# Kernel optimization log

Measured on AMD Instinct MI355X. Metric: run time of the kernel, lower is better.

Reference implementation:

```python
import jax, jax.numpy as jnp
import numpy as np

TOPK = 13
NUM_CLASSES = 80
ALPHA = 1.0
BETA = 6.0
EPS = 1e-9
IOU_EPS = 1e-6  # mmdet BboxOverlaps2D union clamp


def setup_inputs() -> dict:
    key = jax.random.key(0)
    k0, k1, k2, k3, k4 = jax.random.split(key, 5)
    B, G, C = 32, 64, NUM_CLASSES
    # Prior center points for a 640x640 image, strides 8/16/32 -> 8400 priors.
    pts = []
    for s in (8, 16, 32):
        n = 640 // s
        xs = (jnp.arange(n, dtype=jnp.float32) + 0.5) * s
        gy, gx = jnp.meshgrid(xs, xs, indexing='ij')
        pts.append(jnp.stack([gx.ravel(), gy.ravel()], axis=-1))
    priors_points = jnp.concatenate(pts, axis=0)  # [8400, 2]
    P = priors_points.shape[0]
    pred_scores = jax.random.uniform(k0, (B, P, C), dtype=jnp.float32)
    half = jax.random.uniform(k1, (B, P, 2), minval=8.0, maxval=64.0)
    pred_bboxes = jnp.concatenate([priors_points[None] - half,
                                   priors_points[None] + half], axis=-1)
    xy = jax.random.uniform(k2, (B, G, 2), minval=0.0, maxval=560.0)
    wh = jax.random.uniform(k3, (B, G, 2), minval=16.0, maxval=80.0)
    gt_bboxes = jnp.concatenate([xy, xy + wh], axis=-1)
    gt_labels = jax.random.randint(k4, (B, G, 1), 0, C).astype(jnp.int64)
    pad_bbox_flag = jnp.ones((B, G, 1), jnp.float32)
    return {
        'pred_scores': pred_scores,
        'pred_bboxes': pred_bboxes,
        'priors_points': priors_points,
        'gt_labels': gt_labels,
        'gt_bboxes': gt_bboxes,
        'pad_bbox_flag': pad_bbox_flag,
    }


def _pairwise_iou(gt_bboxes, pred_bboxes):
    # gt [B,G,4], pred [B,P,4] (xyxy) -> IoU [B,G,P]
    lt = jnp.maximum(gt_bboxes[:, :, None, :2], pred_bboxes[:, None, :, :2])
    rb = jnp.minimum(gt_bboxes[:, :, None, 2:], pred_bboxes[:, None, :, 2:])
    wh = jnp.clip(rb - lt, 0.0)
    inter = wh[..., 0] * wh[..., 1]
    area_g = (gt_bboxes[..., 2] - gt_bboxes[..., 0]) * (gt_bboxes[..., 3] - gt_bboxes[..., 1])
    area_p = (pred_bboxes[..., 2] - pred_bboxes[..., 0]) * (pred_bboxes[..., 3] - pred_bboxes[..., 1])
    union = area_g[:, :, None] + area_p[:, None, :] - inter
    return inter / jnp.maximum(union, IOU_EPS)


def _assign(pred_scores, pred_bboxes, priors_points, gt_labels, gt_bboxes, pad_bbox_flag):
    B, P, C = pred_scores.shape
    G = gt_bboxes.shape[1]
    labels = gt_labels[..., 0].astype(jnp.int32)  # [B,G]

    # --- box metrics ---
    ps = jnp.swapaxes(pred_scores, 1, 2)  # [B,C,P]
    bbox_scores = ps[jnp.arange(B)[:, None], labels, :]  # [B,G,P]
    overlaps = _pairwise_iou(gt_bboxes, pred_bboxes)      # [B,G,P]
    align = (bbox_scores ** ALPHA) * (overlaps ** BETA)   # [B,G,P]

    # --- candidates inside gt boxes ---
    deltas = jnp.concatenate([
        priors_points[None, None] - gt_bboxes[:, :, None, :2],
        gt_bboxes[:, :, None, 2:] - priors_points[None, None]], axis=-1)  # [B,G,P,4]
    mask_in_gts = (deltas.min(axis=-1) > EPS).astype(align.dtype)  # [B,G,P]

    # --- topk candidate selection ---
    metrics = align * mask_in_gts
    _, topk_idxs = jax.lax.top_k(metrics, TOPK)  # [B,G,TOPK]
    topk_mask = (pad_bbox_flag > 0)              # [B,G,1], broadcasts over TOPK
    topk_idxs = jnp.where(topk_mask, topk_idxs, 0)
    flat_idx = topk_idxs.reshape(B * G, TOPK)
    counts = jnp.zeros((B * G, P), metrics.dtype)
    counts = counts.at[jnp.arange(B * G)[:, None], flat_idx].add(1.0)
    counts = counts.reshape(B, G, P)
    is_in_topk = jnp.where(counts > 1, 0.0, counts)
    pos_mask = is_in_topk * mask_in_gts * pad_bbox_flag  # [B,G,P]

    # --- resolve priors matched to multiple gts: keep highest-IoU gt ---
    fg_mask = pos_mask.sum(axis=1)  # [B,P]
    multi = fg_mask[:, None, :] > 1  # [B,1,P] -> broadcasts to [B,G,P]
    max_ov_idx = overlaps.argmax(axis=1)  # [B,P]
    is_max = jnp.swapaxes(jax.nn.one_hot(max_ov_idx, G, dtype=pos_mask.dtype), 1, 2)  # [B,G,P]
    pos_mask = jnp.where(multi, is_max, pos_mask)
    fg_mask = pos_mask.sum(axis=1)          # [B,P]
    assigned_gt_inds = pos_mask.argmax(axis=1)  # [B,P]

    # --- gather targets ---
    flat_gt = assigned_gt_inds + jnp.arange(B)[:, None] * G  # [B,P]
    assigned_labels = jnp.maximum(labels.reshape(-1)[flat_gt], 0)  # [B,P]
    assigned_bboxes = gt_bboxes.reshape(-1, 4)[flat_gt]            # [B,P,4]
    assigned_scores = jax.nn.one_hot(assigned_labels, C, dtype=pred_scores.dtype)
    assigned_scores = jnp.where((fg_mask > 0)[..., None], assigned_scores, 0.0)

    # --- normalize scores by alignment metric ---
    am = align * pos_mask
    pos_align = am.max(axis=-1, keepdims=True)                 # [B,G,1]
    pos_over = (overlaps * pos_mask).max(axis=-1, keepdims=True)
    norm = (am * pos_over / (pos_align + EPS)).max(axis=1)[..., None]  # [B,P,1]
    assigned_scores = assigned_scores * norm

    return assigned_labels, assigned_bboxes, assigned_scores, fg_mask > 0


def reference(pred_scores, pred_bboxes, priors_points, gt_labels, gt_bboxes, pad_bbox_flag):
    return _assign(pred_scores, pred_bboxes, priors_points, gt_labels, gt_bboxes, pad_bbox_flag)
```

## Files before the change

### kernel.cpp

```cpp
#include <hip/hip_runtime.h>
#include <cstdint>

#pragma clang fp contract(off)

#define B_ 32
#define G_ 64
#define C_ 80
#define P_ 8400
#define TOPK_ 13
#define EPS_IN 1e-9f
#define IOU_EPS_ 1e-6f

typedef unsigned long long u64;
typedef unsigned int u32;

__device__ __forceinline__ float iou_pair(float g0, float g1, float g2, float g3,
                                          float p0, float p1, float p2, float p3) {
    float ix1 = fmaxf(g0, p0);
    float iy1 = fmaxf(g1, p1);
    float ix2 = fminf(g2, p2);
    float iy2 = fminf(g3, p3);
    float iw = fmaxf(ix2 - ix1, 0.0f);
    float ih = fmaxf(iy2 - iy1, 0.0f);
    float inter = iw * ih;
    float ag = (g2 - g0) * (g3 - g1);
    float ap = (p2 - p0) * (p3 - p1);
    float uni = ag + ap - inter;
    return inter / fmaxf(uni, IOU_EPS_);
}

__device__ __forceinline__ float pow6(float x) {
    float x2 = x * x;
    float x4 = x2 * x2;
    return x4 * x2;
}

__global__ __launch_bounds__(256) void topk_kernel(
    const float* __restrict__ pred_scores,
    const float* __restrict__ pred_bboxes,
    const float* __restrict__ priors,
    const int* __restrict__ gt_labels,
    const float* __restrict__ gt_bboxes,
    const float* __restrict__ pad_flag,
    int* __restrict__ cnt,
    int* __restrict__ gsel0)
{
    const int wave = threadIdx.x >> 6;
    const int lane = threadIdx.x & 63;
    const int g = blockIdx.x * 4 + wave;
    const int b = blockIdx.y;
    if (pad_flag[b * G_ + g] <= 0.0f) return;

    const float g0 = gt_bboxes[(b * G_ + g) * 4 + 0];
    const float g1 = gt_bboxes[(b * G_ + g) * 4 + 1];
    const float g2 = gt_bboxes[(b * G_ + g) * 4 + 2];
    const float g3 = gt_bboxes[(b * G_ + g) * 4 + 3];
    int lab = gt_labels[b * G_ + g];
    lab = lab < 0 ? 0 : (lab > C_ - 1 ? C_ - 1 : lab);

    const float4* pb = (const float4*)(pred_bboxes + (size_t)b * P_ * 4);
    const float2* pp = (const float2*)priors;
    const float* ps = pred_scores + (size_t)b * P_ * C_ + lab;

    int x0_[3], y0_[3], nx_[3], c_[3], n_[3] = {80, 40, 20}, base_[3] = {0, 6400, 8000};
    {
        const float invs[3] = {0.125f, 0.0625f, 0.03125f};
#pragma unroll
        for (int l = 0; l < 3; ++l) {
            int n = n_[l];
            int x0 = (int)floorf(g0 * invs[l] - 0.5f) - 1;
            int x1 = (int)ceilf (g2 * invs[l] - 0.5f) + 1;
            int y0 = (int)floorf(g1 * invs[l] - 0.5f) - 1;
            int y1 = (int)ceilf (g3 * invs[l] - 0.5f) + 1;
            x0 = x0 < 0 ? 0 : x0;  y0 = y0 < 0 ? 0 : y0;
            x1 = x1 > n - 1 ? n - 1 : x1;  y1 = y1 > n - 1 ? n - 1 : y1;
            int nx = x1 - x0 + 1, ny = y1 - y0 + 1;
            x0_[l] = x0; y0_[l] = y0;
            nx_[l] = nx > 0 ? nx : 1;
            c_[l] = (nx > 0 && ny > 0) ? nx * ny : 0;
        }
    }
    const int c0 = c_[0], c01 = c_[0] + c_[1], total = c01 + c_[2];

    u64 k0 = 0, k1 = 0, k2 = 0, k3 = 0, k4 = 0, k5 = 0;

    for (int j = lane; j < total; j += 64) {
        int l = (j >= c0) + (j >= c01);
        int r = j - (l == 0 ? 0 : (l == 1 ? c0 : c01));
        int nx = l == 0 ? nx_[0] : (l == 1 ? nx_[1] : nx_[2]);
        int n  = l == 0 ? 80 : (l == 1 ? 40 : 20);
        int bs = l == 0 ? 0 : (l == 1 ? 6400 : 8000);
        int x0 = l == 0 ? x0_[0] : (l == 1 ? x0_[1] : x0_[2]);
        int y0 = l == 0 ? y0_[0] : (l == 1 ? y0_[1] : y0_[2]);
        int iy = r / nx;
        int ix = r - iy * nx;
        int p = bs + (y0 + iy) * n + (x0 + ix);

        float2 pt = pp[p];
        float d0 = pt.x - g0, d1 = pt.y - g1;
        float d2 = g2 - pt.x, d3 = g3 - pt.y;
        float mn = fminf(fminf(d0, d1), fminf(d2, d3));
        if (mn > EPS_IN) {
            float4 box = pb[p];
            float iou = iou_pair(g0, g1, g2, g3, box.x, box.y, box.z, box.w);
            float m = ps[(size_t)p * C_] * pow6(iou);
            u64 key = ((u64)__float_as_uint(m) << 32) | (u32)(~(u32)p);
            bool b0 = key > k0, b1 = key > k1, b2 = key > k2,
                 b3 = key > k3, b4 = key > k4, b5 = key > k5;
            k5 = b4 ? k4 : (b5 ? key : k5);
            k4 = b3 ? k3 : (b4 ? key : k4);
            k3 = b2 ? k2 : (b3 ? key : k3);
            k2 = b1 ? k1 : (b2 ? key : k2);
            k1 = b0 ? k0 : (b1 ? key : k1);
            k0 = b0 ? key : k0;
        }
    }

    u64 mykey = 0;
#pragma unroll
    for (int r = 0; r < TOPK_; ++r) {
        u64 m = k0;
#pragma unroll
        for (int off = 1; off < 64; off <<= 1) {
            u64 o = __shfl_xor(m, off, 64);
            m = o > m ? o : m;
        }
        if (lane == r) mykey = m;
        if (k0 == m && m != 0) {
            k0 = k1; k1 = k2; k2 = k3; k3 = k4; k4 = k5; k5 = 0;
        }
    }

    if (lane < TOPK_ && mykey != 0) {
        int p = (int)(~(u32)mykey);
        atomicAdd(&cnt[b * P_ + p], 1);
        gsel0[b * P_ + p] = g;
    }
}

__global__ __launch_bounds__(256) void assign_kernel(
    const float* __restrict__ pred_scores,
    const float* __restrict__ pred_bboxes,
    const int* __restrict__ gt_labels,
    const float* __restrict__ gt_bboxes,
    const int* __restrict__ cnt,
    int* __restrict__ gsel,
    int* __restrict__ labout,
    float* __restrict__ alignv,
    int* __restrict__ pos_align,
    int* __restrict__ pos_over,
    float* __restrict__ out)
{
    const int b = blockIdx.y;
    const int p = blockIdx.x * 256 + threadIdx.x;
    __shared__ float sgt[G_ * 4];
    __shared__ int slab[G_];
    if (threadIdx.x < G_ * 4) sgt[threadIdx.x] = gt_bboxes[b * G_ * 4 + threadIdx.x];
    if (threadIdx.x < G_) slab[threadIdx.x] = gt_labels[b * G_ + threadIdx.x];
    __syncthreads();
    if (p >= P_) return;

    const int bp = b * P_ + p;
    float4 box = ((const float4*)pred_bboxes)[(size_t)b * P_ + p];

    int c = cnt[bp];
    int g = -1;
    if (c == 1) {
        g = gsel[bp];
    } else if (c > 1) {
        float best = -1.0f;
        int bi = 0;
        for (int gg = 0; gg < G_; ++gg) {
            float v = iou_pair(sgt[gg * 4], sgt[gg * 4 + 1], sgt[gg * 4 + 2], sgt[gg * 4 + 3],
                               box.x, box.y, box.z, box.w);
            if (v > best) { best = v; bi = gg; }
        }
        g = bi;
    }
    gsel[bp] = g;

    const int gu = g < 0 ? 0 : g;
    int labraw = slab[gu];
    int labc = labraw < 0 ? 0 : labraw;

    float* out_lab = out;
    float4* out_bbox = (float4*)(out + (size_t)B_ * P_);
    float* out_fg = out + (size_t)B_ * P_ * (size_t)(1 + 4 + C_);

    out_lab[bp] = (float)labc;
    out_bbox[bp] = make_float4(sgt[gu * 4], sgt[gu * 4 + 1], sgt[gu * 4 + 2], sgt[gu * 4 + 3]);
    out_fg[bp] = g >= 0 ? 1.0f : 0.0f;

    if (g >= 0) {
        float iou = iou_pair(sgt[g * 4], sgt[g * 4 + 1], sgt[g * 4 + 2], sgt[g * 4 + 3],
                             box.x, box.y, box.z, box.w);
        int lb = labc > C_ - 1 ? C_ - 1 : labc;
        float s = pred_scores[(size_t)bp * C_ + lb];
        float al = s * pow6(iou);
        alignv[bp] = al;
        labout[bp] = lb;
        atomicMax(&pos_align[b * G_ + g], __float_as_int(al));
        atomicMax(&pos_over[b * G_ + g], __float_as_int(iou));
    }
}

__global__ __launch_bounds__(256) void scores_fill_kernel(
    const int* __restrict__ gsel,
    const int* __restrict__ labout,
    const float* __restrict__ alignv,
    const int* __restrict__ pos_align,
    const int* __restrict__ pos_over,
    float* __restrict__ out_scores)
{
    int bp = blockIdx.x * 256 + threadIdx.x;
    if (bp >= B_ * P_) return;
    int g = gsel[bp];
    if (g < 0) return;
    int b = bp / P_;
    int bg = b * G_ + g;
    float pa = __int_as_float(pos_align[bg]);
    float po = __int_as_float(pos_over[bg]);
    float val = alignv[bp] * po / (pa + 1e-9f);
    out_scores[(size_t)bp * C_ + labout[bp]] = val;
}

extern "C" void kernel_launch(void* const* d_in, const int* in_sizes, int n_in,
                              void* d_out, int out_size, void* d_ws, size_t ws_size,
                              hipStream_t stream) {
    (void)in_sizes; (void)n_in; (void)out_size; (void)ws_size;
    const float* pred_scores = (const float*)d_in[0];
    const float* pred_bboxes = (const float*)d_in[1];
    const float* priors      = (const float*)d_in[2];
    const int*   gt_labels   = (const int*)d_in[3];
    const float* gt_bboxes   = (const float*)d_in[4];
    const float* pad_flag    = (const float*)d_in[5];
    float* out = (float*)d_out;

    char* ws = (char*)d_ws;
    const size_t BP = (size_t)B_ * P_;
    const size_t BG = (size_t)B_ * G_;
    int* cnt       = (int*)ws;
    int* pos_align = (int*)(ws + BP * 4);
    int* pos_over  = (int*)(ws + BP * 4 + BG * 4);
    int* gsel      = (int*)(ws + BP * 4 + 2 * BG * 4);
    int* labout    = gsel + BP;
    float* alignv  = (float*)(labout + BP);

    hipMemsetAsync(ws, 0, (BP + 2 * BG) * 4, stream);
    hipMemsetAsync(out + BP * 5, 0, BP * (size_t)C_ * 4, stream);

    topk_kernel<<<dim3(G_ / 4, B_), 256, 0, stream>>>(
        pred_scores, pred_bboxes, priors, gt_labels, gt_bboxes, pad_flag, cnt, gsel);

    assign_kernel<<<dim3((P_ + 255) / 256, B_), 256, 0, stream>>>(
        pred_scores, pred_bboxes, gt_labels, gt_bboxes, cnt, gsel, labout, alignv,
        pos_align, pos_over, out);

    scores_fill_kernel<<<(int)((BP + 255) / 256), 256, 0, stream>>>(
        gsel, labout, alignv, pos_align, pos_over, out + BP * 5);
}
```

Measured before the change: 191.7 us.

## Fuse memsets and three kernels into one cooperative kernel with grid syncs

Replaces the two memsets and the three kernel launches with a single cooperative kernel of 512 blocks that zeroes the workspace and score output, runs the per-GT top-k, assigns priors, and fills normalized scores, with grid-wide syncs between phases. Per-prior assignment results are held in registers across the last grid sync instead of being written to and re-read from workspace arrays. The aim is to remove launch and memset overheads and the intermediate global traffic. In exchange it adds grid.sync costs, reads GT boxes from global memory instead of shared memory, and limits parallelism to a fixed grid in the zeroing and top-k phases.

```diff
diff --git a/kernel.cpp b/kernel.cpp
--- a/kernel.cpp
+++ b/kernel.cpp
@@ -1,7 +1,10 @@
 #include <hip/hip_runtime.h>
+#include <hip/hip_cooperative_groups.h>
 #include <cstdint>
 
 #pragma clang fp contract(off)
+
+namespace cg = cooperative_groups;
 
 #define B_ 32
 #define G_ 64
@@ -10,6 +13,8 @@
 #define TOPK_ 13
 #define EPS_IN 1e-9f
 #define IOU_EPS_ 1e-6f
+#define NBLK_ 512
+#define NTHR_ (NBLK_ * 256)
 
 typedef unsigned long long u64;
 typedef unsigned int u32;
@@ -35,7 +40,7 @@
     return x4 * x2;
 }
 
-__global__ __launch_bounds__(256) void topk_kernel(
+__global__ __launch_bounds__(256, 2) void fused_kernel(
     const float* __restrict__ pred_scores,
     const float* __restrict__ pred_bboxes,
     const float* __restrict__ priors,
@@ -43,185 +48,188 @@
     const float* __restrict__ gt_bboxes,
     const float* __restrict__ pad_flag,
     int* __restrict__ cnt,
-    int* __restrict__ gsel0)
-{
-    const int wave = threadIdx.x >> 6;
-    const int lane = threadIdx.x & 63;
-    const int g = blockIdx.x * 4 + wave;
-    const int b = blockIdx.y;
-    if (pad_flag[b * G_ + g] <= 0.0f) return;
-
-    const float g0 = gt_bboxes[(b * G_ + g) * 4 + 0];
-    const float g1 = gt_bboxes[(b * G_ + g) * 4 + 1];
-    const float g2 = gt_bboxes[(b * G_ + g) * 4 + 2];
-    const float g3 = gt_bboxes[(b * G_ + g) * 4 + 3];
-    int lab = gt_labels[b * G_ + g];
-    lab = lab < 0 ? 0 : (lab > C_ - 1 ? C_ - 1 : lab);
-
-    const float4* pb = (const float4*)(pred_bboxes + (size_t)b * P_ * 4);
-    const float2* pp = (const float2*)priors;
-    const float* ps = pred_scores + (size_t)b * P_ * C_ + lab;
-
-    int x0_[3], y0_[3], nx_[3], c_[3], n_[3] = {80, 40, 20}, base_[3] = {0, 6400, 8000};
-    {
-        const float invs[3] = {0.125f, 0.0625f, 0.03125f};
-#pragma unroll
-        for (int l = 0; l < 3; ++l) {
-            int n = n_[l];
-            int x0 = (int)floorf(g0 * invs[l] - 0.5f) - 1;
-            int x1 = (int)ceilf (g2 * invs[l] - 0.5f) + 1;
-            int y0 = (int)floorf(g1 * invs[l] - 0.5f) - 1;
-            int y1 = (int)ceilf (g3 * invs[l] - 0.5f) + 1;
-            x0 = x0 < 0 ? 0 : x0;  y0 = y0 < 0 ? 0 : y0;
-            x1 = x1 > n - 1 ? n - 1 : x1;  y1 = y1 > n - 1 ? n - 1 : y1;
-            int nx = x1 - x0 + 1, ny = y1 - y0 + 1;
-            x0_[l] = x0; y0_[l] = y0;
-            nx_[l] = nx > 0 ? nx : 1;
-            c_[l] = (nx > 0 && ny > 0) ? nx * ny : 0;
-        }
-    }
-    const int c0 = c_[0], c01 = c_[0] + c_[1], total = c01 + c_[2];
-
-    u64 k0 = 0, k1 = 0, k2 = 0, k3 = 0, k4 = 0, k5 = 0;
-
-    for (int j = lane; j < total; j += 64) {
-        int l = (j >= c0) + (j >= c01);
-        int r = j - (l == 0 ? 0 : (l == 1 ? c0 : c01));
-        int nx = l == 0 ? nx_[0] : (l == 1 ? nx_[1] : nx_[2]);
-        int n  = l == 0 ? 80 : (l == 1 ? 40 : 20);
-        int bs = l == 0 ? 0 : (l == 1 ? 6400 : 8000);
-        int x0 = l == 0 ? x0_[0] : (l == 1 ? x0_[1] : x0_[2]);
-        int y0 = l == 0 ? y0_[0] : (l == 1 ? y0_[1] : y0_[2]);
-        int iy = r / nx;
-        int ix = r - iy * nx;
-        int p = bs + (y0 + iy) * n + (x0 + ix);
-
-        float2 pt = pp[p];
-        float d0 = pt.x - g0, d1 = pt.y - g1;
-        float d2 = g2 - pt.x, d3 = g3 - pt.y;
-        float mn = fminf(fminf(d0, d1), fminf(d2, d3));
-        if (mn > EPS_IN) {
-            float4 box = pb[p];
-            float iou = iou_pair(g0, g1, g2, g3, box.x, box.y, box.z, box.w);
-            float m = ps[(size_t)p * C_] * pow6(iou);
-            u64 key = ((u64)__float_as_uint(m) << 32) | (u32)(~(u32)p);
-            bool b0 = key > k0, b1 = key > k1, b2 = key > k2,
-                 b3 = key > k3, b4 = key > k4, b5 = key > k5;
-            k5 = b4 ? k4 : (b5 ? key : k5);
-            k4 = b3 ? k3 : (b4 ? key : k4);
-            k3 = b2 ? k2 : (b3 ? key : k3);
-            k2 = b1 ? k1 : (b2 ? key : k2);
-            k1 = b0 ? k0 : (b1 ? key : k1);
-            k0 = b0 ? key : k0;
-        }
-    }
-
-    u64 mykey = 0;
-#pragma unroll
-    for (int r = 0; r < TOPK_; ++r) {
-        u64 m = k0;
-#pragma unroll
-        for (int off = 1; off < 64; off <<= 1) {
-            u64 o = __shfl_xor(m, off, 64);
-            m = o > m ? o : m;
-        }
-        if (lane == r) mykey = m;
-        if (k0 == m && m != 0) {
-            k0 = k1; k1 = k2; k2 = k3; k3 = k4; k4 = k5; k5 = 0;
-        }
-    }
-
-    if (lane < TOPK_ && mykey != 0) {
-        int p = (int)(~(u32)mykey);
-        atomicAdd(&cnt[b * P_ + p], 1);
-        gsel0[b * P_ + p] = g;
-    }
-}
-
-__global__ __launch_bounds__(256) void assign_kernel(
-    const float* __restrict__ pred_scores,
-    const float* __restrict__ pred_bboxes,
-    const int* __restrict__ gt_labels,
-    const float* __restrict__ gt_bboxes,
-    const int* __restrict__ cnt,
-    int* __restrict__ gsel,
-    int* __restrict__ labout,
-    float* __restrict__ alignv,
+    int* __restrict__ gsel0,
     int* __restrict__ pos_align,
     int* __restrict__ pos_over,
     float* __restrict__ out)
 {
-    const int b = blockIdx.y;
-    const int p = blockIdx.x * 256 + threadIdx.x;
-    __shared__ float sgt[G_ * 4];
-    __shared__ int slab[G_];
-    if (threadIdx.x < G_ * 4) sgt[threadIdx.x] = gt_bboxes[b * G_ * 4 + threadIdx.x];
-    if (threadIdx.x < G_) slab[threadIdx.x] = gt_labels[b * G_ + threadIdx.x];
-    __syncthreads();
-    if (p >= P_) return;
-
-    const int bp = b * P_ + p;
-    float4 box = ((const float4*)pred_bboxes)[(size_t)b * P_ + p];
-
-    int c = cnt[bp];
-    int g = -1;
-    if (c == 1) {
-        g = gsel[bp];
-    } else if (c > 1) {
-        float best = -1.0f;
-        int bi = 0;
-        for (int gg = 0; gg < G_; ++gg) {
-            float v = iou_pair(sgt[gg * 4], sgt[gg * 4 + 1], sgt[gg * 4 + 2], sgt[gg * 4 + 3],
-                               box.x, box.y, box.z, box.w);
-            if (v > best) { best = v; bi = gg; }
+    cg::grid_group grid = cg::this_grid();
+    const int tid = blockIdx.x * 256 + threadIdx.x;
+    const size_t BP = (size_t)B_ * P_;
+
+    {
+        int4* z = (int4*)cnt;
+        const int nz = (B_ * P_ + 2 * B_ * G_) / 4;
+        int4 i0 = make_int4(0, 0, 0, 0);
+        for (int i = tid; i < nz; i += NTHR_) z[i] = i0;
+        float4* zs = (float4*)(out + BP * 5);
+        const int ns = B_ * P_ * (C_ / 4);
+        float4 f0 = make_float4(0.f, 0.f, 0.f, 0.f);
+        for (int i = tid; i < ns; i += NTHR_) zs[i] = f0;
+    }
+    grid.sync();
+
+    {
+        const int waveId = tid >> 6;
+        const int lane = tid & 63;
+        const int b = waveId >> 6;
+        const int g = waveId & 63;
+        if (pad_flag[b * G_ + g] > 0.0f) {
+            const float g0 = gt_bboxes[(b * G_ + g) * 4 + 0];
+            const float g1 = gt_bboxes[(b * G_ + g) * 4 + 1];
+            const float g2 = gt_bboxes[(b * G_ + g) * 4 + 2];
+            const float g3 = gt_bboxes[(b * G_ + g) * 4 + 3];
+            int lab = gt_labels[b * G_ + g];
+            lab = lab < 0 ? 0 : (lab > C_ - 1 ? C_ - 1 : lab);
+
+            const float4* pb = (const float4*)(pred_bboxes + (size_t)b * P_ * 4);
+            const float2* pp = (const float2*)priors;
+            const float* ps = pred_scores + (size_t)b * P_ * C_ + lab;
+
+            int x0_[3], y0_[3], nx_[3], c_[3];
+            {
+                const float invs[3] = {0.125f, 0.0625f, 0.03125f};
+                const int nn[3] = {80, 40, 20};
+#pragma unroll
+                for (int l = 0; l < 3; ++l) {
+                    int n = nn[l];
+                    int x0 = (int)floorf(g0 * invs[l] - 0.5f) - 1;
+                    int x1 = (int)ceilf (g2 * invs[l] - 0.5f) + 1;
+                    int y0 = (int)floorf(g1 * invs[l] - 0.5f) - 1;
+                    int y1 = (int)ceilf (g3 * invs[l] - 0.5f) + 1;
+                    x0 = x0 < 0 ? 0 : x0;  y0 = y0 < 0 ? 0 : y0;
+                    x1 = x1 > n - 1 ? n - 1 : x1;  y1 = y1 > n - 1 ? n - 1 : y1;
+                    int nx = x1 - x0 + 1, ny = y1 - y0 + 1;
+                    x0_[l] = x0; y0_[l] = y0;
+                    nx_[l] = nx > 0 ? nx : 1;
+                    c_[l] = (nx > 0 && ny > 0) ? nx * ny : 0;
+                }
+            }
+            const int c0 = c_[0], c01 = c_[0] + c_[1], total = c01 + c_[2];
+
+            u64 k0 = 0, k1 = 0, k2 = 0, k3 = 0, k4 = 0, k5 = 0;
+
+            for (int j = lane; j < total; j += 64) {
+                int l = (j >= c0) + (j >= c01);
+                int r = j - (l == 0 ? 0 : (l == 1 ? c0 : c01));
+                int nx = l == 0 ? nx_[0] : (l == 1 ? nx_[1] : nx_[2]);
+                int n  = l == 0 ? 80 : (l == 1 ? 40 : 20);
+                int bs = l == 0 ? 0 : (l == 1 ? 6400 : 8000);
+                int x0 = l == 0 ? x0_[0] : (l == 1 ? x0_[1] : x0_[2]);
+                int y0 = l == 0 ? y0_[0] : (l == 1 ? y0_[1] : y0_[2]);
+                int iy = r / nx;
+                int ix = r - iy * nx;
+                int p = bs + (y0 + iy) * n + (x0 + ix);
+
+                float2 pt = pp[p];
+                float d0 = pt.x - g0, d1 = pt.y - g1;
+                float d2 = g2 - pt.x, d3 = g3 - pt.y;
+                float mn = fminf(fminf(d0, d1), fminf(d2, d3));
+                if (mn > EPS_IN) {
+                    float4 box = pb[p];
+                    float iou = iou_pair(g0, g1, g2, g3, box.x, box.y, box.z, box.w);
+                    float m = ps[(size_t)p * C_] * pow6(iou);
+                    u64 key = ((u64)__float_as_uint(m) << 32) | (u32)(~(u32)p);
+                    bool b0 = key > k0, b1 = key > k1, b2 = key > k2,
+                         b3 = key > k3, b4 = key > k4, b5 = key > k5;
+                    k5 = b4 ? k4 : (b5 ? key : k5);
+                    k4 = b3 ? k3 : (b4 ? key : k4);
+                    k3 = b2 ? k2 : (b3 ? key : k3);
+                    k2 = b1 ? k1 : (b2 ? key : k2);
+                    k1 = b0 ? k0 : (b1 ? key : k1);
+                    k0 = b0 ? key : k0;
+                }
+            }
+
+            u64 mykey = 0;
+#pragma unroll
+            for (int r = 0; r < TOPK_; ++r) {
+                u64 m = k0;
+#pragma unroll
+                for (int off = 1; off < 64; off <<= 1) {
+                    u64 o = __shfl_xor(m, off, 64);
+                    m = o > m ? o : m;
+                }
+                if (lane == r) mykey = m;
+                if (k0 == m && m != 0) {
+                    k0 = k1; k1 = k2; k2 = k3; k3 = k4; k4 = k5; k5 = 0;
+                }
+            }
+
+            if (lane < TOPK_ && mykey != 0) {
+                int p = (int)(~(u32)mykey);
+                atomicAdd(&cnt[b * P_ + p], 1);
+                gsel0[b * P_ + p] = g;
+            }
         }
-        g = bi;
-    }
-    gsel[bp] = g;
-
-    const int gu = g < 0 ? 0 : g;
-    int labraw = slab[gu];
-    int labc = labraw < 0 ? 0 : labraw;
-
-    float* out_lab = out;
-    float4* out_bbox = (float4*)(out + (size_t)B_ * P_);
-    float* out_fg = out + (size_t)B_ * P_ * (size_t)(1 + 4 + C_);
-
-    out_lab[bp] = (float)labc;
-    out_bbox[bp] = make_float4(sgt[gu * 4], sgt[gu * 4 + 1], sgt[gu * 4 + 2], sgt[gu * 4 + 3]);
-    out_fg[bp] = g >= 0 ? 1.0f : 0.0f;
-
-    if (g >= 0) {
-        float iou = iou_pair(sgt[g * 4], sgt[g * 4 + 1], sgt[g * 4 + 2], sgt[g * 4 + 3],
-                             box.x, box.y, box.z, box.w);
-        int lb = labc > C_ - 1 ? C_ - 1 : labc;
-        float s = pred_scores[(size_t)bp * C_ + lb];
-        float al = s * pow6(iou);
-        alignv[bp] = al;
-        labout[bp] = lb;
-        atomicMax(&pos_align[b * G_ + g], __float_as_int(al));
-        atomicMax(&pos_over[b * G_ + g], __float_as_int(iou));
-    }
-}
-
-__global__ __launch_bounds__(256) void scores_fill_kernel(
-    const int* __restrict__ gsel,
-    const int* __restrict__ labout,
-    const float* __restrict__ alignv,
-    const int* __restrict__ pos_align,
-    const int* __restrict__ pos_over,
-    float* __restrict__ out_scores)
-{
-    int bp = blockIdx.x * 256 + threadIdx.x;
-    if (bp >= B_ * P_) return;
-    int g = gsel[bp];
-    if (g < 0) return;
-    int b = bp / P_;
-    int bg = b * G_ + g;
-    float pa = __int_as_float(pos_align[bg]);
-    float po = __int_as_float(pos_over[bg]);
-    float val = alignv[bp] * po / (pa + 1e-9f);
-    out_scores[(size_t)bp * C_ + labout[bp]] = val;
+    }
+    grid.sync();
+
+    int resg0 = -1, resg1 = -1, resg2 = -1;
+    int reslab0 = 0, reslab1 = 0, reslab2 = 0;
+    float resal0 = 0.f, resal1 = 0.f, resal2 = 0.f;
+#pragma unroll
+    for (int it = 0; it < 3; ++it) {
+        int bp = tid + it * NTHR_;
+        if (bp < (int)BP) {
+            int b = bp / P_;
+            const float4* gtb = (const float4*)(gt_bboxes + (size_t)b * G_ * 4);
+            float4 box = ((const float4*)pred_bboxes)[bp];
+
+            int c = cnt[bp];
+            int g = -1;
+            if (c == 1) {
+                g = gsel0[bp];
+            } else if (c > 1) {
+                float best = -1.0f;
+                int bi = 0;
+                for (int gg = 0; gg < G_; ++gg) {
+                    float4 gb = gtb[gg];
+                    float v = iou_pair(gb.x, gb.y, gb.z, gb.w, box.x, box.y, box.z, box.w);
+                    if (v > best) { best = v; bi = gg; }
+                }
+                g = bi;
+            }
+
+            int gu = g < 0 ? 0 : g;
+            float4 gb = gtb[gu];
+            int labraw = gt_labels[b * G_ + gu];
+            int labc = labraw < 0 ? 0 : labraw;
+
+            out[bp] = (float)labc;
+            ((float4*)(out + BP))[bp] = gb;
+            out[BP * 85 + bp] = g >= 0 ? 1.0f : 0.0f;
+
+            if (g >= 0) {
+                float iou = iou_pair(gb.x, gb.y, gb.z, gb.w, box.x, box.y, box.z, box.w);
+                int lb = labc > C_ - 1 ? C_ - 1 : labc;
+                float s = pred_scores[(size_t)bp * C_ + lb];
+                float al = s * pow6(iou);
+                int bg = b * G_ + g;
+                atomicMax(&pos_align[bg], __float_as_int(al));
+                atomicMax(&pos_over[bg], __float_as_int(iou));
+                if (it == 0) { resg0 = g; reslab0 = lb; resal0 = al; }
+                else if (it == 1) { resg1 = g; reslab1 = lb; resal1 = al; }
+                else { resg2 = g; reslab2 = lb; resal2 = al; }
+            }
+        }
+    }
+    grid.sync();
+
+#pragma unroll
+    for (int it = 0; it < 3; ++it) {
+        int g = it == 0 ? resg0 : (it == 1 ? resg1 : resg2);
+        if (g >= 0) {
+            int bp = tid + it * NTHR_;
+            int lb = it == 0 ? reslab0 : (it == 1 ? reslab1 : reslab2);
+            float al = it == 0 ? resal0 : (it == 1 ? resal1 : resal2);
+            int b = bp / P_;
+            int bg = b * G_ + g;
+            float pa = __int_as_float(pos_align[bg]);
+            float po = __int_as_float(pos_over[bg]);
+            out[BP * 5 + (size_t)bp * C_ + lb] = al * po / (pa + 1e-9f);
+        }
+    }
 }
 
 extern "C" void kernel_launch(void* const* d_in, const int* in_sizes, int n_in,
@@ -236,26 +244,17 @@
     const float* pad_flag    = (const float*)d_in[5];
     float* out = (float*)d_out;
 
-    char* ws = (char*)d_ws;
-    const size_t BP = (size_t)B_ * P_;
-    const size_t BG = (size_t)B_ * G_;
-    int* cnt       = (int*)ws;
-    int* pos_align = (int*)(ws + BP * 4);
-    int* pos_over  = (int*)(ws + BP * 4 + BG * 4);
-    int* gsel      = (int*)(ws + BP * 4 + 2 * BG * 4);
-    int* labout    = gsel + BP;
-    float* alignv  = (float*)(labout + BP);
-
-    hipMemsetAsync(ws, 0, (BP + 2 * BG) * 4, stream);
-    hipMemsetAsync(out + BP * 5, 0, BP * (size_t)C_ * 4, stream);
-
-    topk_kernel<<<dim3(G_ / 4, B_), 256, 0, stream>>>(
-        pred_scores, pred_bboxes, priors, gt_labels, gt_bboxes, pad_flag, cnt, gsel);
-
-    assign_kernel<<<dim3((P_ + 255) / 256, B_), 256, 0, stream>>>(
-        pred_scores, pred_bboxes, gt_labels, gt_bboxes, cnt, gsel, labout, alignv,
-        pos_align, pos_over, out);
-
-    scores_fill_kernel<<<(int)((BP + 255) / 256), 256, 0, stream>>>(
-        gsel, labout, alignv, pos_align, pos_over, out + BP * 5);
-}
+    int* cnt       = (int*)d_ws;
+    int* pos_align = cnt + (size_t)B_ * P_;
+    int* pos_over  = pos_align + (size_t)B_ * G_;
+    int* gsel0     = pos_over + (size_t)B_ * G_;
+
+    void* args[] = {
+        (void*)&pred_scores, (void*)&pred_bboxes, (void*)&priors,
+        (void*)&gt_labels, (void*)&gt_bboxes, (void*)&pad_flag,
+        (void*)&cnt, (void*)&gsel0, (void*)&pos_align, (void*)&pos_over,
+        (void*)&out
+    };
+    hipLaunchCooperativeKernel((const void*)fused_kernel,
+                               dim3(NBLK_), dim3(256), args, 0, stream);
+}
```

Measured after the change: 371.3 us. 93.6% more time.
